# Kernel tuning notes

Hardware: AMD Instinct MI355X
Metric: run time of the kernel (lower is better)

The kernel has to match this reference:

```python
import jax, jax.numpy as jnp
import numpy as np

N = 50000        # num nodes
E = 1_600_000    # num edges
NNZ = 16         # sparse features per node
V = 100000       # feature vocabulary (num_total_features)
D = 128          # embedding_dim
H = 128          # hidden_dim
O = 64           # out_embedding_dim


def setup_inputs() -> dict:
    key = jax.random.key(0)
    ks = jax.random.split(key, 12)
    s = 0.05
    return {
        "feature_indices": jax.random.randint(ks[0], (N * NNZ,), 0, V, dtype=jnp.int32),
        "feature_offsets": jnp.arange(N, dtype=jnp.int32) * NNZ,
        "feature_weights": jax.random.uniform(ks[1], (N * NNZ,), dtype=jnp.float32),
        "edge_index": jax.random.randint(ks[2], (2, E), 0, N, dtype=jnp.int32),
        "noise": jax.random.normal(ks[3], (N, O), dtype=jnp.float32),
        "emb_table": jax.random.normal(ks[4], (V, D), dtype=jnp.float32) * s,
        "W1": jax.random.normal(ks[5], (D, H), dtype=jnp.float32) * s,
        "b1": jnp.zeros((H,), dtype=jnp.float32),
        "Wmu": jax.random.normal(ks[6], (H, O), dtype=jnp.float32) * s,
        "bmu": jnp.zeros((O,), dtype=jnp.float32),
        "Wls": jax.random.normal(ks[7], (H, O), dtype=jnp.float32) * s,
        "bls": jnp.zeros((O,), dtype=jnp.float32),
    }


def _gcn(x, W, b, src, dst, norm_e, deg_inv):
    # GCNConv with self-loops and symmetric normalization:
    # out_i = sum_{j->i} norm_ji * (W x_j) + deg_i^{-1} * (W x_i) + b
    xw = x @ W
    agg = jax.ops.segment_sum(norm_e[:, None] * xw[src], dst, num_segments=N)
    return agg + xw * deg_inv[:, None] + b


def reference(feature_indices, feature_offsets, feature_weights, edge_index, noise,
              emb_table, W1, b1, Wmu, bmu, Wls, bls):
    # --- EmbeddingBag(mode='sum') with per_sample_weights ---
    total = feature_indices.shape[0]
    bag_ids = jnp.searchsorted(feature_offsets, jnp.arange(total), side="right") - 1
    x = jax.ops.segment_sum(feature_weights[:, None] * emb_table[feature_indices],
                            bag_ids, num_segments=N)  # [N, D]
    # --- F.normalize(p=2, dim=-1) ---
    x = x / jnp.maximum(jnp.linalg.norm(x, axis=-1, keepdims=True), 1e-12)

    # --- shared GCN normalization (self-loops added) ---
    src, dst = edge_index[0], edge_index[1]
    deg = 1.0 + jax.ops.segment_sum(jnp.ones((E,), x.dtype), dst, num_segments=N)
    deg_isqrt = deg ** -0.5
    norm_e = deg_isqrt[src] * deg_isqrt[dst]  # per-edge norm
    deg_inv = 1.0 / deg                        # self-loop norm

    # --- encoder ---
    h = jax.nn.relu(_gcn(x, W1, b1, src, dst, norm_e, deg_inv))
    mu = _gcn(h, Wmu, bmu, src, dst, norm_e, deg_inv)
    logstd = _gcn(h, Wls, bls, src, dst, norm_e, deg_inv)
    z = mu + noise * jnp.exp(logstd)

    # --- dot-product decoder over edge_index ---
    logits = jnp.sum(z[src] * z[dst], axis=-1)  # [E]
    return logits
```

## Files before the change

### kernel.cpp

```cpp
#include <hip/hip_runtime.h>
#include <hip/hip_bf16.h>

constexpr int N_ = 50000;
constexpr int E_ = 1600000;
constexpr int D_ = 128;
constexpr int O_ = 64;
constexpr int NNZ_ = 16;
constexpr int V_ = 100000;
constexpr int NBIN_ = (N_ + 255) / 256;

static __device__ __forceinline__ unsigned short f2bf(float f) {
    __hip_bfloat16 h = __float2bfloat16(f);
    return __builtin_bit_cast(unsigned short, h);
}
static __device__ __forceinline__ float blo(unsigned int u) { return __uint_as_float(u << 16); }
static __device__ __forceinline__ float bhi(unsigned int u) { return __uint_as_float(u & 0xffff0000u); }
static __device__ __forceinline__ float4 fma4(float s, float4 a, float4 b) {
    return make_float4(fmaf(s, a.x, b.x), fmaf(s, a.y, b.y),
                       fmaf(s, a.z, b.z), fmaf(s, a.w, b.w));
}

__global__ __launch_bounds__(256) void k_cvt(const float* __restrict__ emb,
                                             unsigned int* __restrict__ emb_bf) {
    int t = blockIdx.x * blockDim.x + threadIdx.x;
    if (t >= V_ * D_ / 8) return;
    float4 a = ((const float4*)emb)[t * 2];
    float4 b = ((const float4*)emb)[t * 2 + 1];
    uint4 o;
    o.x = (unsigned int)f2bf(a.x) | ((unsigned int)f2bf(a.y) << 16);
    o.y = (unsigned int)f2bf(a.z) | ((unsigned int)f2bf(a.w) << 16);
    o.z = (unsigned int)f2bf(b.x) | ((unsigned int)f2bf(b.y) << 16);
    o.w = (unsigned int)f2bf(b.z) | ((unsigned int)f2bf(b.w) << 16);
    ((uint4*)emb_bf)[t] = o;
}

__global__ __launch_bounds__(256) void k_embed(const int* __restrict__ fi,
                                               const float* __restrict__ fw,
                                               const unsigned int* __restrict__ emb_bf,
                                               unsigned int* __restrict__ x) {
    int n = blockIdx.x * 4 + (threadIdx.x >> 6);
    if (n >= N_) return;
    int lane = threadIdx.x & 63;
    float a0 = 0.f, a1 = 0.f;
    int base = n * NNZ_;
#pragma unroll
    for (int j = 0; j < NNZ_; ++j) {
        int idx  = fi[base + j];
        float w  = fw[base + j];
        unsigned int r = emb_bf[(size_t)idx * 64 + lane];
        a0 = fmaf(w, blo(r), a0);
        a1 = fmaf(w, bhi(r), a1);
    }
    float ss = a0 * a0 + a1 * a1;
#pragma unroll
    for (int o = 32; o; o >>= 1) ss += __shfl_xor(ss, o);
    float sc = 1.0f / fmaxf(sqrtf(ss), 1e-12f);
    x[(size_t)n * 64 + lane] =
        (unsigned int)f2bf(a0 * sc) | ((unsigned int)f2bf(a1 * sc) << 16);
}

constexpr int EPB_ = 4096;
__global__ __launch_bounds__(256) void k_bhist(const int* __restrict__ dst,
                                               int* __restrict__ bin_total) {
    __shared__ int hist[256];
    int t = threadIdx.x;
    hist[t] = 0;
    __syncthreads();
    int e0 = blockIdx.x * EPB_;
#pragma unroll
    for (int i = 0; i < EPB_ / 256; ++i) {
        int e = e0 + i * 256 + t;
        if (e < E_) atomicAdd(&hist[dst[e] >> 8], 1);
    }
    __syncthreads();
    if (t < NBIN_ && hist[t]) atomicAdd(&bin_total[t], hist[t]);
}

__global__ __launch_bounds__(256) void k_scan196(const int* __restrict__ bin_total,
                                                 int* __restrict__ coarse_start,
                                                 int* __restrict__ coarse_cursor,
                                                 int* __restrict__ row_start) {
    __shared__ int s[256];
    int t = threadIdx.x;
    int v = (t < NBIN_) ? bin_total[t] : 0;
    s[t] = v;
    __syncthreads();
    for (int o = 1; o < 256; o <<= 1) {
        int u = (t >= o) ? s[t - o] : 0;
        __syncthreads();
        s[t] += u;
        __syncthreads();
    }
    int excl = s[t] - v;
    if (t <= NBIN_) { coarse_start[t] = excl; coarse_cursor[t] = excl; }
    if (t == 0) row_start[N_] = E_;
}

__global__ __launch_bounds__(256) void k_bin(const int* __restrict__ src,
                                             const int* __restrict__ dst,
                                             int* __restrict__ coarse_cursor,
                                             unsigned int* __restrict__ binned) {
    __shared__ int hist[256], base[256];
    int t = threadIdx.x;
    int e0 = blockIdx.x * EPB_;
    hist[t] = 0;
    __syncthreads();
#pragma unroll
    for (int i = 0; i < EPB_ / 256; ++i) {
        int e = e0 + i * 256 + t;
        if (e < E_) atomicAdd(&hist[dst[e] >> 8], 1);
    }
    __syncthreads();
    if (t < NBIN_ && hist[t]) base[t] = atomicAdd(&coarse_cursor[t], hist[t]);
    __syncthreads();
#pragma unroll
    for (int i = 0; i < EPB_ / 256; ++i) {
        int e = e0 + i * 256 + t;
        if (e < E_) {
            int d = dst[e];
            int pos = atomicAdd(&base[d >> 8], 1);
            binned[pos] = (unsigned int)src[e] | ((unsigned int)(d & 255) << 16);
        }
    }
}

__global__ __launch_bounds__(256) void k_node(const unsigned int* __restrict__ binned,
                                              const int* __restrict__ coarse_start,
                                              float* __restrict__ disq,
                                              float* __restrict__ dinv,
                                              int* __restrict__ row_start) {
    __shared__ int hist[256], s[256];
    int t = threadIdx.x;
    hist[t] = 0;
    __syncthreads();
    int beg = coarse_start[blockIdx.x], end = coarse_start[blockIdx.x + 1];
    for (int j = beg + t; j < end; j += 256)
        atomicAdd(&hist[(binned[j] >> 16) & 255], 1);
    __syncthreads();
    int v = hist[t];
    int n = (blockIdx.x << 8) + t;
    if (n < N_) {
        float deg = 1.0f + (float)v;
        disq[n] = rsqrtf(deg);
        dinv[n] = 1.0f / deg;
    }
    s[t] = v;
    __syncthreads();
    for (int o = 1; o < 256; o <<= 1) {
        int u = (t >= o) ? s[t - o] : 0;
        __syncthreads();
        s[t] += u;
        __syncthreads();
    }
    if (n < N_) row_start[n] = beg + (s[t] - v);
}

__global__ __launch_bounds__(256) void k_fill2(const unsigned int* __restrict__ binned,
                                               const int* __restrict__ coarse_start,
                                               const int* __restrict__ row_start,
                                               int* __restrict__ sorted_src) {
    __shared__ int cur[256];
    int t = threadIdx.x;
    int n0 = blockIdx.x << 8;
    if (n0 + t < N_) cur[t] = row_start[n0 + t];
    __syncthreads();
    int beg = coarse_start[blockIdx.x], end = coarse_start[blockIdx.x + 1];
    for (int j = beg + t; j < end; j += 256) {
        unsigned int b = binned[j];
        int pos = atomicAdd(&cur[(b >> 16) & 255], 1);
        sorted_src[pos] = (int)(b & 0xFFFFu);
    }
}

__global__ __launch_bounds__(256) void k_gather(const int* __restrict__ row_start,
                                                const int* __restrict__ sorted_src,
                                                const float* __restrict__ disq,
                                                const float* __restrict__ dinv,
                                                const unsigned int* __restrict__ v,
                                                float* __restrict__ agg) {
    int n = blockIdx.x * 4 + (threadIdx.x >> 6);
    if (n >= N_) return;
    int lane = threadIdx.x & 63;
    int beg = row_start[n], end = row_start[n + 1];
    float ax = 0.f, ay = 0.f;
    int j = beg;
    for (; j + 7 < end; j += 8) {
        int s0 = sorted_src[j],     s1 = sorted_src[j + 1];
        int s2 = sorted_src[j + 2], s3 = sorted_src[j + 3];
        int s4 = sorted_src[j + 4], s5 = sorted_src[j + 5];
        int s6 = sorted_src[j + 6], s7 = sorted_src[j + 7];
        float w0 = disq[s0], w1 = disq[s1], w2 = disq[s2], w3 = disq[s3];
        float w4 = disq[s4], w5 = disq[s5], w6 = disq[s6], w7 = disq[s7];
        unsigned int b0 = v[(size_t)s0 * 64 + lane];
        unsigned int b1 = v[(size_t)s1 * 64 + lane];
        unsigned int b2 = v[(size_t)s2 * 64 + lane];
        unsigned int b3 = v[(size_t)s3 * 64 + lane];
        unsigned int b4 = v[(size_t)s4 * 64 + lane];
        unsigned int b5 = v[(size_t)s5 * 64 + lane];
        unsigned int b6 = v[(size_t)s6 * 64 + lane];
        unsigned int b7 = v[(size_t)s7 * 64 + lane];
        ax = fmaf(w0, blo(b0), ax); ay = fmaf(w0, bhi(b0), ay);
        ax = fmaf(w1, blo(b1), ax); ay = fmaf(w1, bhi(b1), ay);
        ax = fmaf(w2, blo(b2), ax); ay = fmaf(w2, bhi(b2), ay);
        ax = fmaf(w3, blo(b3), ax); ay = fmaf(w3, bhi(b3), ay);
        ax = fmaf(w4, blo(b4), ax); ay = fmaf(w4, bhi(b4), ay);
        ax = fmaf(w5, blo(b5), ax); ay = fmaf(w5, bhi(b5), ay);
        ax = fmaf(w6, blo(b6), ax); ay = fmaf(w6, bhi(b6), ay);
        ax = fmaf(w7, blo(b7), ax); ay = fmaf(w7, bhi(b7), ay);
    }
    for (; j < end; ++j) {
        int s = sorted_src[j];
        float w = disq[s];
        unsigned int b = v[(size_t)s * 64 + lane];
        ax = fmaf(w, blo(b), ax); ay = fmaf(w, bhi(b), ay);
    }
    float dq = disq[n], di = dinv[n];
    unsigned int bs = v[(size_t)n * 64 + lane];
    ax = fmaf(di, blo(bs), ax * dq);
    ay = fmaf(di, bhi(bs), ay * dq);
    ((float2*)agg)[(size_t)n * 64 + lane] = make_float2(ax, ay);
}

__global__ __launch_bounds__(256, 2) void k_gemm_relu(const float* __restrict__ u,
                                                      const float* __restrict__ W,
                                                      const float* __restrict__ b,
                                                      unsigned short* __restrict__ hout) {
    __shared__ float lw[D_ * D_];
    __shared__ float lu[32 * D_];
    int tid = threadIdx.x;
    for (int t = tid; t < D_ * D_ / 4; t += 256)
        ((float4*)lw)[t] = ((const float4*)W)[t];

    int l  = tid & 31;
    int rl = ((tid >> 6) << 3) + (((tid >> 5) & 1) << 2);
    float4 bb = ((const float4*)b)[l];

    for (int tile = blockIdx.x; tile * 32 < N_; tile += gridDim.x) {
        int row0 = tile * 32;
        __syncthreads();
#pragma unroll
        for (int i = 0; i < 4; ++i) {
            int flat = i * 256 + tid;
            int r = flat >> 5, c4 = flat & 31;
            int gr = row0 + r;
            ((float4*)lu)[flat] = (gr < N_) ? ((const float4*)u)[(size_t)gr * 32 + c4]
                                            : make_float4(0.f, 0.f, 0.f, 0.f);
        }
        __syncthreads();
        float4 a0 = {0,0,0,0}, a1 = {0,0,0,0}, a2 = {0,0,0,0}, a3 = {0,0,0,0};
#pragma unroll 4
        for (int k4 = 0; k4 < 32; ++k4) {
            int k = k4 * 4;
            float4 w0 = ((const float4*)(lw + (k + 0) * D_))[l];
            float4 w1 = ((const float4*)(lw + (k + 1) * D_))[l];
            float4 w2 = ((const float4*)(lw + (k + 2) * D_))[l];
            float4 w3 = ((const float4*)(lw + (k + 3) * D_))[l];
            float4 u0 = ((const float4*)(lu + (rl + 0) * D_))[k4];
            float4 u1 = ((const float4*)(lu + (rl + 1) * D_))[k4];
            float4 u2 = ((const float4*)(lu + (rl + 2) * D_))[k4];
            float4 u3 = ((const float4*)(lu + (rl + 3) * D_))[k4];
            a0 = fma4(u0.x, w0, fma4(u0.y, w1, fma4(u0.z, w2, fma4(u0.w, w3, a0))));
            a1 = fma4(u1.x, w0, fma4(u1.y, w1, fma4(u1.z, w2, fma4(u1.w, w3, a1))));
            a2 = fma4(u2.x, w0, fma4(u2.y, w1, fma4(u2.z, w2, fma4(u2.w, w3, a2))));
            a3 = fma4(u3.x, w0, fma4(u3.y, w1, fma4(u3.z, w2, fma4(u3.w, w3, a3))));
        }
        float4 accs[4] = {a0, a1, a2, a3};
#pragma unroll
        for (int r = 0; r < 4; ++r) {
            int row = row0 + rl + r;
            if (row < N_) {
                float4 a = accs[r];
                ushort4 o;
                o.x = f2bf(fmaxf(a.x + bb.x, 0.f));
                o.y = f2bf(fmaxf(a.y + bb.y, 0.f));
                o.z = f2bf(fmaxf(a.z + bb.z, 0.f));
                o.w = f2bf(fmaxf(a.w + bb.w, 0.f));
                ((ushort4*)hout)[(size_t)row * 32 + l] = o;
            }
        }
    }
}

__global__ __launch_bounds__(256, 2) void k_gemm_z(const float* __restrict__ g,
                                                   const float* __restrict__ Wmu,
                                                   const float* __restrict__ bmu,
                                                   const float* __restrict__ Wls,
                                                   const float* __restrict__ bls,
                                                   const float* __restrict__ noise,
                                                   unsigned int* __restrict__ z) {
    __shared__ float lw[D_ * D_];
    __shared__ float lu[32 * D_];
    int tid = threadIdx.x;
    for (int t = tid; t < D_ * 32; t += 256) {
        int k = t >> 5, j2 = t & 31;
        float2 m2 = ((const float2*)Wmu)[k * 32 + j2];
        float2 l2 = ((const float2*)Wls)[k * 32 + j2];
        ((float4*)lw)[t] = make_float4(m2.x, l2.x, m2.y, l2.y);
    }

    int l  = tid & 31;
    int rl = ((tid >> 6) << 3) + (((tid >> 5) & 1) << 2);
    float2 bm = ((const float2*)bmu)[l];
    float2 bl = ((const float2*)bls)[l];
    float4 bb = make_float4(bm.x, bl.x, bm.y, bl.y);

    for (int tile = blockIdx.x; tile * 32 < N_; tile += gridDim.x) {
        int row0 = tile * 32;
        __syncthreads();
#pragma unroll
        for (int i = 0; i < 4; ++i) {
            int flat = i * 256 + tid;
            int r = flat >> 5, c4 = flat & 31;
            int gr = row0 + r;
            ((float4*)lu)[flat] = (gr < N_) ? ((const float4*)g)[(size_t)gr * 32 + c4]
                                            : make_float4(0.f, 0.f, 0.f, 0.f);
        }
        __syncthreads();
        float4 a0 = {0,0,0,0}, a1 = {0,0,0,0}, a2 = {0,0,0,0}, a3 = {0,0,0,0};
#pragma unroll 4
        for (int k4 = 0; k4 < 32; ++k4) {
            int k = k4 * 4;
            float4 w0 = ((const float4*)(lw + (k + 0) * D_))[l];
            float4 w1 = ((const float4*)(lw + (k + 1) * D_))[l];
            float4 w2 = ((const float4*)(lw + (k + 2) * D_))[l];
            float4 w3 = ((const float4*)(lw + (k + 3) * D_))[l];
            float4 u0 = ((const float4*)(lu + (rl + 0) * D_))[k4];
            float4 u1 = ((const float4*)(lu + (rl + 1) * D_))[k4];
            float4 u2 = ((const float4*)(lu + (rl + 2) * D_))[k4];
            float4 u3 = ((const float4*)(lu + (rl + 3) * D_))[k4];
            a0 = fma4(u0.x, w0, fma4(u0.y, w1, fma4(u0.z, w2, fma4(u0.w, w3, a0))));
            a1 = fma4(u1.x, w0, fma4(u1.y, w1, fma4(u1.z, w2, fma4(u1.w, w3, a1))));
            a2 = fma4(u2.x, w0, fma4(u2.y, w1, fma4(u2.z, w2, fma4(u2.w, w3, a2))));
            a3 = fma4(u3.x, w0, fma4(u3.y, w1, fma4(u3.z, w2, fma4(u3.w, w3, a3))));
        }
        float4 accs[4] = {a0, a1, a2, a3};
#pragma unroll
        for (int r = 0; r < 4; ++r) {
            int row = row0 + rl + r;
            if (row < N_) {
                float4 a = accs[r];
                float2 n2 = ((const float2*)noise)[(size_t)row * 32 + l];
                float z0 = (a.x + bb.x) + n2.x * expf(a.y + bb.y);
                float z1 = (a.z + bb.z) + n2.y * expf(a.w + bb.w);
                z[(size_t)row * 32 + l] =
                    (unsigned int)f2bf(z0) | ((unsigned int)f2bf(z1) << 16);
            }
        }
    }
}

__global__ __launch_bounds__(256) void k_decode(const int* __restrict__ src,
                                                const int* __restrict__ dst,
                                                const unsigned int* __restrict__ z,
                                                float* __restrict__ out) {
    int e = blockIdx.x * 16 + (threadIdx.x >> 4);
    if (e >= E_) return;
    int l = threadIdx.x & 15;
    int s = src[e], d = dst[e];
    uint2 za = ((const uint2*)z)[(size_t)s * 16 + l];
    uint2 zb = ((const uint2*)z)[(size_t)d * 16 + l];
    float p = blo(za.x) * blo(zb.x) + bhi(za.x) * bhi(zb.x)
            + blo(za.y) * blo(zb.y) + bhi(za.y) * bhi(zb.y);
#pragma unroll
    for (int o = 8; o; o >>= 1) p += __shfl_xor(p, o);
    if (l == 0) out[e] = p;
}

extern "C" void kernel_launch(void* const* d_in, const int* in_sizes, int n_in,
                              void* d_out, int out_size, void* d_ws, size_t ws_size,
                              hipStream_t stream) {
    const int*   fi    = (const int*)d_in[0];
    const float* fw    = (const float*)d_in[2];
    const int*   ei    = (const int*)d_in[3];
    const float* noise = (const float*)d_in[4];
    const float* emb   = (const float*)d_in[5];
    const float* W1    = (const float*)d_in[6];
    const float* b1    = (const float*)d_in[7];
    const float* Wmu   = (const float*)d_in[8];
    const float* bmu   = (const float*)d_in[9];
    const float* Wls   = (const float*)d_in[10];
    const float* bls   = (const float*)d_in[11];
    float* out = (float*)d_out;

    const int* src = ei;
    const int* dst = ei + E_;

    float*        ws        = (float*)d_ws;
    float*        agg       = ws;
    unsigned int* emb_bf    = (unsigned int*)agg;
    unsigned int* binned    = (unsigned int*)agg;
    unsigned int* x         = (unsigned int*)(agg + (size_t)N_ * D_);
    unsigned int* h         = x + (size_t)N_ * 64;
    unsigned int* z         = h + (size_t)N_ * 64;
    float*        disq      = (float*)(z + (size_t)N_ * 32);
    float*        dinv      = disq + N_;
    int*          row_start = (int*)(dinv + N_);
    int*          sorted_src= row_start + (N_ + 1);
    int*          bin_total = sorted_src + E_;
    int*          coarse_start  = bin_total + 256;
    int*          coarse_cursor = coarse_start + 256;

    hipMemsetAsync(bin_total, 0, 256 * sizeof(int), stream);

    k_cvt    <<<(V_ * D_ / 8 + 255) / 256, 256, 0, stream>>>(emb, emb_bf);
    k_embed  <<<N_ / 4,                 256, 0, stream>>>(fi, fw, emb_bf, x);
    k_bhist  <<<(E_ + EPB_ - 1) / EPB_, 256, 0, stream>>>(dst, bin_total);
    k_scan196<<<1,                      256, 0, stream>>>(bin_total, coarse_start,
                                                          coarse_cursor, row_start);
    k_bin    <<<(E_ + EPB_ - 1) / EPB_, 256, 0, stream>>>(src, dst, coarse_cursor, binned);
    k_node   <<<NBIN_,                  256, 0, stream>>>(binned, coarse_start,
                                                          disq, dinv, row_start);
    k_fill2  <<<NBIN_,                  256, 0, stream>>>(binned, coarse_start,
                                                          row_start, sorted_src);

    k_gather   <<<N_ / 4, 256, 0, stream>>>(row_start, sorted_src, disq, dinv, x, agg);
    k_gemm_relu<<<512,    256, 0, stream>>>(agg, W1, b1, (unsigned short*)h);

    k_gather <<<N_ / 4,   256, 0, stream>>>(row_start, sorted_src, disq, dinv, h, agg);
    k_gemm_z <<<512,      256, 0, stream>>>(agg, Wmu, bmu, Wls, bls, noise, z);

    k_decode <<<E_ / 16,  256, 0, stream>>>(src, dst, z, out);
}
```

Baseline: 489.8 us.

## Widen gathers to 8-byte loads, store aggregates in bf16, vectorize decode

The embedding and neighbor-gather kernels now use 32 lanes with uint2 loads per row. In the gather, each half-wavefront handles alternate edges and the halves are combined with a cross-half shuffle. The aggregated features are written as bf16 rather than fp32, halving the intermediate traffic, and the GEMM loaders unpack them. Decode now uses 8 lanes with uint4 loads and processes two edges per 8-lane group. The goal is fewer, wider memory transactions and less bandwidth, at the cost of extra bf16 rounding on the aggregates.

```diff
diff --git a/kernel.cpp b/kernel.cpp
--- a/kernel.cpp
+++ b/kernel.cpp
@@ -13,6 +13,9 @@
     __hip_bfloat16 h = __float2bfloat16(f);
     return __builtin_bit_cast(unsigned short, h);
 }
+static __device__ __forceinline__ unsigned int pack2(float a, float b) {
+    return (unsigned int)f2bf(a) | ((unsigned int)f2bf(b) << 16);
+}
 static __device__ __forceinline__ float blo(unsigned int u) { return __uint_as_float(u << 16); }
 static __device__ __forceinline__ float bhi(unsigned int u) { return __uint_as_float(u & 0xffff0000u); }
 static __device__ __forceinline__ float4 fma4(float s, float4 a, float4 b) {
@@ -27,10 +30,10 @@
     float4 a = ((const float4*)emb)[t * 2];
     float4 b = ((const float4*)emb)[t * 2 + 1];
     uint4 o;
-    o.x = (unsigned int)f2bf(a.x) | ((unsigned int)f2bf(a.y) << 16);
-    o.y = (unsigned int)f2bf(a.z) | ((unsigned int)f2bf(a.w) << 16);
-    o.z = (unsigned int)f2bf(b.x) | ((unsigned int)f2bf(b.y) << 16);
-    o.w = (unsigned int)f2bf(b.z) | ((unsigned int)f2bf(b.w) << 16);
+    o.x = pack2(a.x, a.y);
+    o.y = pack2(a.z, a.w);
+    o.z = pack2(b.x, b.y);
+    o.w = pack2(b.z, b.w);
     ((uint4*)emb_bf)[t] = o;
 }
 
@@ -38,25 +41,28 @@
                                                const float* __restrict__ fw,
                                                const unsigned int* __restrict__ emb_bf,
                                                unsigned int* __restrict__ x) {
-    int n = blockIdx.x * 4 + (threadIdx.x >> 6);
+    int lane = threadIdx.x & 63;
+    int h = lane >> 5, c = lane & 31;
+    int n = blockIdx.x * 8 + ((threadIdx.x >> 6) << 1) + h;
     if (n >= N_) return;
-    int lane = threadIdx.x & 63;
-    float a0 = 0.f, a1 = 0.f;
+    float a0 = 0.f, a1 = 0.f, a2 = 0.f, a3 = 0.f;
     int base = n * NNZ_;
 #pragma unroll
     for (int j = 0; j < NNZ_; ++j) {
         int idx  = fi[base + j];
         float w  = fw[base + j];
-        unsigned int r = emb_bf[(size_t)idx * 64 + lane];
-        a0 = fmaf(w, blo(r), a0);
-        a1 = fmaf(w, bhi(r), a1);
-    }
-    float ss = a0 * a0 + a1 * a1;
-#pragma unroll
-    for (int o = 32; o; o >>= 1) ss += __shfl_xor(ss, o);
+        uint2 r = ((const uint2*)emb_bf)[(size_t)idx * 32 + c];
+        a0 = fmaf(w, blo(r.x), a0);
+        a1 = fmaf(w, bhi(r.x), a1);
+        a2 = fmaf(w, blo(r.y), a2);
+        a3 = fmaf(w, bhi(r.y), a3);
+    }
+    float ss = a0 * a0 + a1 * a1 + a2 * a2 + a3 * a3;
+#pragma unroll
+    for (int o = 16; o; o >>= 1) ss += __shfl_xor(ss, o);
     float sc = 1.0f / fmaxf(sqrtf(ss), 1e-12f);
-    x[(size_t)n * 64 + lane] =
-        (unsigned int)f2bf(a0 * sc) | ((unsigned int)f2bf(a1 * sc) << 16);
+    ((uint2*)x)[(size_t)n * 32 + c] =
+        make_uint2(pack2(a0 * sc, a1 * sc), pack2(a2 * sc, a3 * sc));
 }
 
 constexpr int EPB_ = 4096;
@@ -177,51 +183,53 @@
                                                 const float* __restrict__ disq,
                                                 const float* __restrict__ dinv,
                                                 const unsigned int* __restrict__ v,
-                                                float* __restrict__ agg) {
+                                                unsigned int* __restrict__ agg) {
     int n = blockIdx.x * 4 + (threadIdx.x >> 6);
     if (n >= N_) return;
     int lane = threadIdx.x & 63;
+    int h = lane >> 5, c = lane & 31;
+    const uint2* V = (const uint2*)v;
     int beg = row_start[n], end = row_start[n + 1];
-    float ax = 0.f, ay = 0.f;
+    float a0 = 0.f, a1 = 0.f, a2 = 0.f, a3 = 0.f;
     int j = beg;
     for (; j + 7 < end; j += 8) {
-        int s0 = sorted_src[j],     s1 = sorted_src[j + 1];
-        int s2 = sorted_src[j + 2], s3 = sorted_src[j + 3];
-        int s4 = sorted_src[j + 4], s5 = sorted_src[j + 5];
-        int s6 = sorted_src[j + 6], s7 = sorted_src[j + 7];
+        int s0 = sorted_src[j     + h], s1 = sorted_src[j + 2 + h];
+        int s2 = sorted_src[j + 4 + h], s3 = sorted_src[j + 6 + h];
         float w0 = disq[s0], w1 = disq[s1], w2 = disq[s2], w3 = disq[s3];
-        float w4 = disq[s4], w5 = disq[s5], w6 = disq[s6], w7 = disq[s7];
-        unsigned int b0 = v[(size_t)s0 * 64 + lane];
-        unsigned int b1 = v[(size_t)s1 * 64 + lane];
-        unsigned int b2 = v[(size_t)s2 * 64 + lane];
-        unsigned int b3 = v[(size_t)s3 * 64 + lane];
-        unsigned int b4 = v[(size_t)s4 * 64 + lane];
-        unsigned int b5 = v[(size_t)s5 * 64 + lane];
-        unsigned int b6 = v[(size_t)s6 * 64 + lane];
-        unsigned int b7 = v[(size_t)s7 * 64 + lane];
-        ax = fmaf(w0, blo(b0), ax); ay = fmaf(w0, bhi(b0), ay);
-        ax = fmaf(w1, blo(b1), ax); ay = fmaf(w1, bhi(b1), ay);
-        ax = fmaf(w2, blo(b2), ax); ay = fmaf(w2, bhi(b2), ay);
-        ax = fmaf(w3, blo(b3), ax); ay = fmaf(w3, bhi(b3), ay);
-        ax = fmaf(w4, blo(b4), ax); ay = fmaf(w4, bhi(b4), ay);
-        ax = fmaf(w5, blo(b5), ax); ay = fmaf(w5, bhi(b5), ay);
-        ax = fmaf(w6, blo(b6), ax); ay = fmaf(w6, bhi(b6), ay);
-        ax = fmaf(w7, blo(b7), ax); ay = fmaf(w7, bhi(b7), ay);
-    }
-    for (; j < end; ++j) {
-        int s = sorted_src[j];
+        uint2 b0 = V[(size_t)s0 * 32 + c];
+        uint2 b1 = V[(size_t)s1 * 32 + c];
+        uint2 b2 = V[(size_t)s2 * 32 + c];
+        uint2 b3 = V[(size_t)s3 * 32 + c];
+        a0 = fmaf(w0, blo(b0.x), a0); a1 = fmaf(w0, bhi(b0.x), a1);
+        a2 = fmaf(w0, blo(b0.y), a2); a3 = fmaf(w0, bhi(b0.y), a3);
+        a0 = fmaf(w1, blo(b1.x), a0); a1 = fmaf(w1, bhi(b1.x), a1);
+        a2 = fmaf(w1, blo(b1.y), a2); a3 = fmaf(w1, bhi(b1.y), a3);
+        a0 = fmaf(w2, blo(b2.x), a0); a1 = fmaf(w2, bhi(b2.x), a1);
+        a2 = fmaf(w2, blo(b2.y), a2); a3 = fmaf(w2, bhi(b2.y), a3);
+        a0 = fmaf(w3, blo(b3.x), a0); a1 = fmaf(w3, bhi(b3.x), a1);
+        a2 = fmaf(w3, blo(b3.y), a2); a3 = fmaf(w3, bhi(b3.y), a3);
+    }
+    for (; j + h < end; j += 2) {
+        int s = sorted_src[j + h];
         float w = disq[s];
-        unsigned int b = v[(size_t)s * 64 + lane];
-        ax = fmaf(w, blo(b), ax); ay = fmaf(w, bhi(b), ay);
-    }
-    float dq = disq[n], di = dinv[n];
-    unsigned int bs = v[(size_t)n * 64 + lane];
-    ax = fmaf(di, blo(bs), ax * dq);
-    ay = fmaf(di, bhi(bs), ay * dq);
-    ((float2*)agg)[(size_t)n * 64 + lane] = make_float2(ax, ay);
-}
-
-__global__ __launch_bounds__(256, 2) void k_gemm_relu(const float* __restrict__ u,
+        uint2 b = V[(size_t)s * 32 + c];
+        a0 = fmaf(w, blo(b.x), a0); a1 = fmaf(w, bhi(b.x), a1);
+        a2 = fmaf(w, blo(b.y), a2); a3 = fmaf(w, bhi(b.y), a3);
+    }
+    a0 += __shfl_xor(a0, 32); a1 += __shfl_xor(a1, 32);
+    a2 += __shfl_xor(a2, 32); a3 += __shfl_xor(a3, 32);
+    if (h == 0) {
+        float dq = disq[n], di = dinv[n];
+        uint2 bs = V[(size_t)n * 32 + c];
+        a0 = fmaf(di, blo(bs.x), a0 * dq);
+        a1 = fmaf(di, bhi(bs.x), a1 * dq);
+        a2 = fmaf(di, blo(bs.y), a2 * dq);
+        a3 = fmaf(di, bhi(bs.y), a3 * dq);
+        ((uint2*)agg)[(size_t)n * 32 + c] = make_uint2(pack2(a0, a1), pack2(a2, a3));
+    }
+}
+
+__global__ __launch_bounds__(256, 2) void k_gemm_relu(const unsigned int* __restrict__ ub,
                                                       const float* __restrict__ W,
                                                       const float* __restrict__ b,
                                                       unsigned short* __restrict__ hout) {
@@ -239,12 +247,13 @@
         int row0 = tile * 32;
         __syncthreads();
 #pragma unroll
-        for (int i = 0; i < 4; ++i) {
-            int flat = i * 256 + tid;
-            int r = flat >> 5, c4 = flat & 31;
+        for (int i = 0; i < 8; ++i) {
+            int t = i * 256 + tid;
+            int r = t >> 6, slot = t & 63;
             int gr = row0 + r;
-            ((float4*)lu)[flat] = (gr < N_) ? ((const float4*)u)[(size_t)gr * 32 + c4]
-                                            : make_float4(0.f, 0.f, 0.f, 0.f);
+            unsigned int bv = (gr < N_) ? ub[(size_t)gr * 64 + slot] : 0u;
+            lu[r * D_ + slot * 2]     = blo(bv);
+            lu[r * D_ + slot * 2 + 1] = bhi(bv);
         }
         __syncthreads();
         float4 a0 = {0,0,0,0}, a1 = {0,0,0,0}, a2 = {0,0,0,0}, a3 = {0,0,0,0};
@@ -281,7 +290,7 @@
     }
 }
 
-__global__ __launch_bounds__(256, 2) void k_gemm_z(const float* __restrict__ g,
+__global__ __launch_bounds__(256, 2) void k_gemm_z(const unsigned int* __restrict__ gb,
                                                    const float* __restrict__ Wmu,
                                                    const float* __restrict__ bmu,
                                                    const float* __restrict__ Wls,
@@ -308,12 +317,13 @@
         int row0 = tile * 32;
         __syncthreads();
 #pragma unroll
-        for (int i = 0; i < 4; ++i) {
-            int flat = i * 256 + tid;
-            int r = flat >> 5, c4 = flat & 31;
+        for (int i = 0; i < 8; ++i) {
+            int t = i * 256 + tid;
+            int r = t >> 6, slot = t & 63;
             int gr = row0 + r;
-            ((float4*)lu)[flat] = (gr < N_) ? ((const float4*)g)[(size_t)gr * 32 + c4]
-                                            : make_float4(0.f, 0.f, 0.f, 0.f);
+            unsigned int bv = (gr < N_) ? gb[(size_t)gr * 64 + slot] : 0u;
+            lu[r * D_ + slot * 2]     = blo(bv);
+            lu[r * D_ + slot * 2 + 1] = bhi(bv);
         }
         __syncthreads();
         float4 a0 = {0,0,0,0}, a1 = {0,0,0,0}, a2 = {0,0,0,0}, a3 = {0,0,0,0};
@@ -342,8 +352,7 @@
                 float2 n2 = ((const float2*)noise)[(size_t)row * 32 + l];
                 float z0 = (a.x + bb.x) + n2.x * expf(a.y + bb.y);
                 float z1 = (a.z + bb.z) + n2.y * expf(a.w + bb.w);
-                z[(size_t)row * 32 + l] =
-                    (unsigned int)f2bf(z0) | ((unsigned int)f2bf(z1) << 16);
+                z[(size_t)row * 32 + l] = pack2(z0, z1);
             }
         }
     }
@@ -353,17 +362,32 @@
                                                 const int* __restrict__ dst,
                                                 const unsigned int* __restrict__ z,
                                                 float* __restrict__ out) {
-    int e = blockIdx.x * 16 + (threadIdx.x >> 4);
-    if (e >= E_) return;
-    int l = threadIdx.x & 15;
-    int s = src[e], d = dst[e];
-    uint2 za = ((const uint2*)z)[(size_t)s * 16 + l];
-    uint2 zb = ((const uint2*)z)[(size_t)d * 16 + l];
-    float p = blo(za.x) * blo(zb.x) + bhi(za.x) * bhi(zb.x)
-            + blo(za.y) * blo(zb.y) + bhi(za.y) * bhi(zb.y);
-#pragma unroll
-    for (int o = 8; o; o >>= 1) p += __shfl_xor(p, o);
-    if (l == 0) out[e] = p;
+    int l = threadIdx.x & 7;
+    int e0 = blockIdx.x * 64 + ((threadIdx.x >> 3) << 1);
+    int s0 = src[e0], d0 = dst[e0];
+    int s1 = src[e0 + 1], d1 = dst[e0 + 1];
+    const uint4* Z = (const uint4*)z;
+    uint4 za0 = Z[(size_t)s0 * 8 + l];
+    uint4 zb0 = Z[(size_t)d0 * 8 + l];
+    uint4 za1 = Z[(size_t)s1 * 8 + l];
+    uint4 zb1 = Z[(size_t)d1 * 8 + l];
+    float p0 = blo(za0.x) * blo(zb0.x) + bhi(za0.x) * bhi(zb0.x)
+             + blo(za0.y) * blo(zb0.y) + bhi(za0.y) * bhi(zb0.y)
+             + blo(za0.z) * blo(zb0.z) + bhi(za0.z) * bhi(zb0.z)
+             + blo(za0.w) * blo(zb0.w) + bhi(za0.w) * bhi(zb0.w);
+    float p1 = blo(za1.x) * blo(zb1.x) + bhi(za1.x) * bhi(zb1.x)
+             + blo(za1.y) * blo(zb1.y) + bhi(za1.y) * bhi(zb1.y)
+             + blo(za1.z) * blo(zb1.z) + bhi(za1.z) * bhi(zb1.z)
+             + blo(za1.w) * blo(zb1.w) + bhi(za1.w) * bhi(zb1.w);
+#pragma unroll
+    for (int o = 4; o; o >>= 1) {
+        p0 += __shfl_xor(p0, o);
+        p1 += __shfl_xor(p1, o);
+    }
+    if (l == 0) {
+        out[e0]     = p0;
+        out[e0 + 1] = p1;
+    }
 }
 
 extern "C" void kernel_launch(void* const* d_in, const int* in_sizes, int n_in,
@@ -386,10 +410,10 @@
     const int* dst = ei + E_;
 
     float*        ws        = (float*)d_ws;
-    float*        agg       = ws;
-    unsigned int* emb_bf    = (unsigned int*)agg;
-    unsigned int* binned    = (unsigned int*)agg;
-    unsigned int* x         = (unsigned int*)(agg + (size_t)N_ * D_);
+    unsigned int* aggb      = (unsigned int*)ws;
+    unsigned int* emb_bf    = (unsigned int*)ws;
+    unsigned int* binned    = (unsigned int*)ws;
+    unsigned int* x         = (unsigned int*)ws + (size_t)V_ * 64;
     unsigned int* h         = x + (size_t)N_ * 64;
     unsigned int* z         = h + (size_t)N_ * 64;
     float*        disq      = (float*)(z + (size_t)N_ * 32);
@@ -403,7 +427,7 @@
     hipMemsetAsync(bin_total, 0, 256 * sizeof(int), stream);
 
     k_cvt    <<<(V_ * D_ / 8 + 255) / 256, 256, 0, stream>>>(emb, emb_bf);
-    k_embed  <<<N_ / 4,                 256, 0, stream>>>(fi, fw, emb_bf, x);
+    k_embed  <<<(N_ + 7) / 8,           256, 0, stream>>>(fi, fw, emb_bf, x);
     k_bhist  <<<(E_ + EPB_ - 1) / EPB_, 256, 0, stream>>>(dst, bin_total);
     k_scan196<<<1,                      256, 0, stream>>>(bin_total, coarse_start,
                                                           coarse_cursor, row_start);
@@ -413,11 +437,11 @@
     k_fill2  <<<NBIN_,                  256, 0, stream>>>(binned, coarse_start,
                                                           row_start, sorted_src);
 
-    k_gather   <<<N_ / 4, 256, 0, stream>>>(row_start, sorted_src, disq, dinv, x, agg);
-    k_gemm_relu<<<512,    256, 0, stream>>>(agg, W1, b1, (unsigned short*)h);
-
-    k_gather <<<N_ / 4,   256, 0, stream>>>(row_start, sorted_src, disq, dinv, h, agg);
-    k_gemm_z <<<512,      256, 0, stream>>>(agg, Wmu, bmu, Wls, bls, noise, z);
-
-    k_decode <<<E_ / 16,  256, 0, stream>>>(src, dst, z, out);
-}
+    k_gather   <<<N_ / 4, 256, 0, stream>>>(row_start, sorted_src, disq, dinv, x, aggb);
+    k_gemm_relu<<<512,    256, 0, stream>>>(aggb, W1, b1, (unsigned short*)h);
+
+    k_gather <<<N_ / 4,   256, 0, stream>>>(row_start, sorted_src, disq, dinv, h, aggb);
+    k_gemm_z <<<512,      256, 0, stream>>>(aggb, Wmu, bmu, Wls, bls, noise, z);
+
+    k_decode <<<E_ / 64,  256, 0, stream>>>(src, dst, z, out);
+}
```

Measured after the change: 449.3 us. 1.09x faster.
